# Performance work log

Hardware: AMD Instinct MI355X
Metric: run time of the kernel (lower is better)

Reference implementation:

```python
import jax, jax.numpy as jnp
import numpy as np

N, E = 50000, 800000
IN_C, H_C, OUT_C, HEADS = 64, 32, 32, 8


def setup_inputs() -> dict:
    key = jax.random.key(0)
    ks = jax.random.split(key, 16)
    def glorot(k, shape):
        fan_in = shape[-1]
        return jax.random.normal(k, shape, dtype=jnp.float32) / jnp.sqrt(jnp.float32(fan_in))
    inp = {
        'x': jax.random.normal(ks[0], (N, IN_C), dtype=jnp.float32),
        'edge_index': jax.random.randint(ks[1], (2, E), 0, N, dtype=jnp.int64),
        # layer 1: in_c -> h_c, heads
        'W1l': glorot(ks[2], (HEADS * H_C, IN_C)),
        'b1l': jnp.zeros((HEADS * H_C,), jnp.float32),
        'W1r': glorot(ks[3], (HEADS * H_C, IN_C)),
        'b1r': jnp.zeros((HEADS * H_C,), jnp.float32),
        'att1': glorot(ks[4], (HEADS, H_C)),
        'bias1': jnp.zeros((H_C,), jnp.float32),
        # layer 2: h_c -> out_c, heads
        'W2l': glorot(ks[5], (HEADS * OUT_C, H_C)),
        'b2l': jnp.zeros((HEADS * OUT_C,), jnp.float32),
        'W2r': glorot(ks[6], (HEADS * OUT_C, H_C)),
        'b2r': jnp.zeros((HEADS * OUT_C,), jnp.float32),
        'att2': glorot(ks[7], (HEADS, OUT_C)),
        'bias2': jnp.zeros((OUT_C,), jnp.float32),
    }
    return inp


def _gatv2_layer(x, src, dst, valid, Wl, bl, Wr, br, att, bias):
    # PyG GATv2Conv (share_weights=False, concat=False): message j->i uses
    # e = att . leaky_relu(lin_l(x_j) + lin_r(x_i), 0.2); softmax over dst; agg lin_l(x_j).
    n = x.shape[0]
    heads, c = att.shape
    xl = (x @ Wl.T + bl).reshape(n, heads, c)
    xr = (x @ Wr.T + br).reshape(n, heads, c)
    m = jax.nn.leaky_relu(xl[src] + xr[dst], negative_slope=0.2)  # [Etot,H,C]
    score = jnp.einsum('ehc,hc->eh', m, att)                      # [Etot,H]
    score = jnp.where(valid[:, None], score, -jnp.inf)
    smax = jax.ops.segment_max(score, dst, num_segments=n)        # [N,H]
    a = jnp.where(valid[:, None], jnp.exp(score - smax[dst]), 0.0)
    denom = jax.ops.segment_sum(a, dst, num_segments=n)
    a = a / jnp.maximum(denom[dst], 1e-16)
    out = jax.ops.segment_sum(a[..., None] * xl[src], dst, num_segments=n)  # [N,H,C]
    return out.mean(axis=1) + bias


def reference(x, edge_index, W1l, b1l, W1r, b1r, att1, bias1,
              W2l, b2l, W2r, b2r, att2, bias2):
    n = x.shape[0]
    src0, dst0 = edge_index[0], edge_index[1]
    # PyG removes existing self loops then adds fresh ones: mask originals,
    # append one self loop per node (keeps static shapes).
    loop = jnp.arange(n, dtype=src0.dtype)
    src = jnp.concatenate([src0, loop])
    dst = jnp.concatenate([dst0, loop])
    valid = jnp.concatenate([src0 != dst0, jnp.ones((n,), bool)])
    h = _gatv2_layer(x, src, dst, valid, W1l, b1l, W1r, b1r, att1, bias1)
    h = jax.nn.leaky_relu(h, negative_slope=0.01)  # nn.LeakyReLU default
    out = _gatv2_layer(h, src, dst, valid, W2l, b2l, W2r, b2r, att2, bias2)
    return out
```

## Files before the change

kernel.cpp:

```cpp
#include <hip/hip_runtime.h>
#include <math.h>

#define HEADS 8
#define CDIM 32
#define ODIM 256
#define BKT_SHIFT 7
#define CHUNK 2048

typedef _Float16 h2 __attribute__((ext_vector_type(2)));
typedef _Float16 h4 __attribute__((ext_vector_type(4)));
typedef _Float16 h8 __attribute__((ext_vector_type(8)));
typedef float f32x4 __attribute__((ext_vector_type(4)));
typedef unsigned long long u64;
union H4 { h4 v; h2 p[2]; u64 u; };

#if __has_builtin(__builtin_amdgcn_fdot2)
#define FDOT2(a,b,c) __builtin_amdgcn_fdot2((a),(b),(c),false)
#else
static __device__ __forceinline__ float fdot2_sw(h2 a, h2 b, float c){
  return fmaf((float)a.x, (float)b.x, fmaf((float)a.y, (float)b.y, c));
}
#define FDOT2(a,b,c) fdot2_sw((a),(b),(c))
#endif

__device__ __forceinline__ float lrelu(float v, float s){ return fmaxf(v, s*v); }

__global__ __launch_bounds__(256) void wcvt_kernel(
    const float* __restrict__ W1l, const float* __restrict__ W1r,
    const float* __restrict__ W2l, const float* __restrict__ W2r,
    _Float16* __restrict__ w1lh, _Float16* __restrict__ w1rh,
    _Float16* __restrict__ w2lh, _Float16* __restrict__ w2rh){
  int i = (blockIdx.x*256 + threadIdx.x)*4;
  const float* s; _Float16* d; int off;
  if (i < 16384)      { s = W1l; d = w1lh; off = i; }
  else if (i < 32768) { s = W1r; d = w1rh; off = i - 16384; }
  else if (i < 40960) { s = W2l; d = w2lh; off = i - 32768; }
  else                { s = W2r; d = w2rh; off = i - 40960; }
  float4 v = *(const float4*)(s + off);
  *(h4*)(d + off) = (h4){(_Float16)v.x, (_Float16)v.y, (_Float16)v.z, (_Float16)v.w};
}


__global__ __launch_bounds__(512) void csr_offs_kernel(
    int* __restrict__ hist, int* __restrict__ btotal, int NB, int B){
  __shared__ int s[512];
  int b = blockIdx.x, t = threadIdx.x;
  int v = (t < NB) ? hist[t*B + b] : 0;
  s[t] = v;
  __syncthreads();
  for (int off=1; off<512; off<<=1){
    int u = (t >= off) ? s[t-off] : 0;
    __syncthreads(); s[t] += u; __syncthreads();
  }
  int excl = s[t] - v;
  if (t < NB) hist[t*B + b] = excl;
  if (t == NB-1) btotal[b] = excl + v;
}

__global__ __launch_bounds__(512) void csr_base_kernel(
    const int* __restrict__ btotal, int* __restrict__ base, int B){
  __shared__ int s[512];
  int t = threadIdx.x;
  int v = (t < B) ? btotal[t] : 0;
  s[t] = v;
  __syncthreads();
  for (int off=1; off<512; off<<=1){
    int u = (t >= off) ? s[t-off] : 0;
    __syncthreads(); s[t] += u; __syncthreads();
  }
  if (t < B) base[t] = s[t] - v;
  if (t == B-1) base[B] = s[t];
}

__global__ __launch_bounds__(256) void csr_scatter_kernel(
    const int* __restrict__ src, const int* __restrict__ dst,
    const int* __restrict__ rank, const int* __restrict__ offs,
    const int* __restrict__ base, int* __restrict__ bpack, int e, int B){
  int t = threadIdx.x, k = blockIdx.x;
  int base_i = k*CHUNK;
#pragma unroll
  for (int j = 0; j < CHUNK/256; ++j){
    int i = base_i + j*256 + t;
    if (i < e){
      int r = rank[i];
      if (r >= 0){
        int d = dst[i], s = src[i];
        int b = d >> BKT_SHIFT;
        int pos = base[b] + offs[k*B + b] + r;
        bpack[pos] = (s << BKT_SHIFT) | (d & 127);
      }
    }
  }
}

__global__ __launch_bounds__(256) void csr_sort_kernel(
    const int* __restrict__ bpack, const int* __restrict__ base,
    int* __restrict__ csr, int* __restrict__ indptr, int n, int B){
  __shared__ int lh[128], cur[128], ss[128];
  int b = blockIdx.x, t = threadIdx.x;
  int beg = base[b], cnt = base[b+1] - beg;
  if (t < 128) lh[t] = 0;
  __syncthreads();
  for (int j = t; j < cnt; j += 256){
    int p = bpack[beg + j];
    atomicAdd(&lh[p & 127], 1);
  }
  __syncthreads();
  int v = (t < 128) ? lh[t] : 0;
  if (t < 128) ss[t] = v;
  __syncthreads();
  for (int off=1; off<128; off<<=1){
    int u = (t >= off && t < 128) ? ss[t-off] : 0;
    __syncthreads();
    if (t < 128) ss[t] += u;
    __syncthreads();
  }
  if (t < 128){
    int excl = ss[t] - v;
    cur[t] = excl;
    int node = (b << BKT_SHIFT) + t;
    if (node <= n) indptr[node] = beg + excl;
  }
  __syncthreads();
  for (int j = t; j < cnt; j += 256){
    int p = bpack[beg + j];
    int lpos = atomicAdd(&cur[p & 127], 1);
    csr[beg + lpos] = p >> BKT_SHIFT;
  }
}

template<int K, bool FUSE_HIST>
__global__ __launch_bounds__(512) void gemm_mfma(const float* __restrict__ X,
    const _Float16* __restrict__ Wlh, const float* __restrict__ bl,
    const _Float16* __restrict__ Wrh, const float* __restrict__ br,
    _Float16* __restrict__ outl, _Float16* __restrict__ outr, int n,
    const int* __restrict__ src, const int* __restrict__ dst,
    int* __restrict__ rank, int* __restrict__ hist, int e, int B){
  if (FUSE_HIST && blockIdx.y == 1){
    int k = blockIdx.x;
    int NB = (e + CHUNK-1)/CHUNK;
    if (k >= NB) return;
    __shared__ int lh[512];
    int t = threadIdx.x;
    if (t < 512) lh[t] = 0;
    __syncthreads();
    int base_i = k*CHUNK;
#pragma unroll
    for (int j = 0; j < CHUNK/512; ++j){
      int i = base_i + j*512 + t;
      if (i < e){
        int s = src[i], d = dst[i];
        int r = -1;
        if (s != d) r = atomicAdd(&lh[d>>BKT_SHIFT], 1);
        rank[i] = r;
      }
    }
    __syncthreads();
    for (int b = t; b < B; b += 512) hist[k*B + b] = lh[b];
    return;
  }
  const int KP = K + 8;
  __shared__ __align__(16) _Float16 Xs[64*(K+8)];
  int t = threadIdx.x;
  int n0 = blockIdx.x*64;

  for (int idx = t; idx < 64*(K/4); idx += 512){
    int row = idx/(K/4), c = (idx%(K/4))*4;
    int node = n0 + row; if (node >= n) node = n-1;
    f32x4 xv = __builtin_nontemporal_load((const f32x4*)(X + (size_t)node*K + c));
    *(h4*)(Xs + row*KP + c) = (h4){(_Float16)xv[0], (_Float16)xv[1],
                                   (_Float16)xv[2], (_Float16)xv[3]};
  }
  __syncthreads();

  int wave = t >> 6, lane = t & 63;
  int co = wave*64;
  const _Float16* W = (co < 256) ? Wlh : Wrh;
  const float* Bv   = (co < 256) ? bl : br;
  _Float16* outp    = (co < 256) ? outl : outr;
  int lco = co & 255;
  int lr = lane & 15, lg = lane >> 4;

  f32x4 acc[4][4];
#pragma unroll
  for (int c = 0; c < 4; ++c)
#pragma unroll
    for (int m = 0; m < 4; ++m) acc[c][m] = (f32x4){0.f, 0.f, 0.f, 0.f};

#pragma unroll
  for (int ks = 0; ks < K/32; ++ks){
    int k0 = ks*32 + lg*8;
    h8 a[4], b[4];
#pragma unroll
    for (int c = 0; c < 4; ++c)
      a[c] = *(const h8*)(W + (size_t)(lco + c*16 + lr)*K + k0);
#pragma unroll
    for (int m = 0; m < 4; ++m)
      b[m] = *(const h8*)(Xs + (m*16 + lr)*KP + k0);
#pragma unroll
    for (int c = 0; c < 4; ++c)
#pragma unroll
      for (int m = 0; m < 4; ++m)
        acc[c][m] = __builtin_amdgcn_mfma_f32_16x16x32_f16(a[c], b[m], acc[c][m], 0, 0, 0);
  }

#pragma unroll
  for (int c = 0; c < 4; ++c){
    int ch = lco + c*16 + lg*4;
    float4 bb = *(const float4*)(Bv + ch);
#pragma unroll
    for (int m = 0; m < 4; ++m){
      int node = n0 + m*16 + lr;
      if (node < n){
        h4 o = {(_Float16)(acc[c][m][0] + bb.x), (_Float16)(acc[c][m][1] + bb.y),
                (_Float16)(acc[c][m][2] + bb.z), (_Float16)(acc[c][m][3] + bb.w)};
        *(h4*)(outp + (size_t)node*ODIM + ch) = o;
      }
    }
  }
}

__global__ __launch_bounds__(256) void edge_kernel(
    const _Float16* __restrict__ xl, const _Float16* __restrict__ xr,
    const float* __restrict__ att, const float* __restrict__ bias,
    const int* __restrict__ indptr, const int* __restrict__ csr_src,
    float* __restrict__ out, int n, int act)
{
  int wid = blockIdx.x*4 + (threadIdx.x >> 6);
  if (wid >= n) return;
  int lane = threadIdx.x & 63;
  const float LOG2E = 1.44269504088896341f;

  float4 attf = *(const float4*)(att + 4*lane);
  h2 at0 = (h2){(_Float16)(attf.x*LOG2E), (_Float16)(attf.y*LOG2E)};
  h2 at1 = (h2){(_Float16)(attf.z*LOG2E), (_Float16)(attf.w*LOG2E)};
  const h2 c02 = {(_Float16)0.2f, (_Float16)0.2f};

  H4 xrh; xrh.u = __builtin_nontemporal_load((const u64*)(xr + (size_t)wid*ODIM + 4*lane));
  H4 self; self.v = *(const h4*)(xl + (size_t)wid*ODIM + 4*lane);

  auto score = [&](const H4& c)->float{
    h2 t0 = c.p[0] + xrh.p[0];
    h2 t1 = c.p[1] + xrh.p[1];
    h2 q0 = __builtin_elementwise_max(t0, t0 * c02);
    h2 q1 = __builtin_elementwise_max(t1, t1 * c02);
    float d = FDOT2(q0, at0, FDOT2(q1, at1, 0.f));
    d += __shfl_xor(d, 1);
    d += __shfl_xor(d, 2);
    d += __shfl_xor(d, 4);
    return d;
  };

  float w0 = exp2f(score(self));
  float denom = w0;
  float4 acc;
  acc.x = w0 * (float)self.v.x;
  acc.y = w0 * (float)self.v.y;
  acc.z = w0 * (float)self.v.z;
  acc.w = w0 * (float)self.v.w;

  int beg = __builtin_amdgcn_readfirstlane(indptr[wid]);
  int end = __builtin_amdgcn_readfirstlane(indptr[wid+1]);
  int cnt = end - beg;

#define GATHER(j) (*(const h4*)(xl + (size_t)((unsigned)__shfl(sidx,(j)))*ODIM + 4*lane))
  for (int cb = 0; cb < cnt; cb += 64){
    int ccnt = min(cnt - cb, 64);
    int sidx = (lane < ccnt) ? __builtin_nontemporal_load(csr_src + beg + cb + lane) : 0;
    H4 r0, r1, r2, r3;
    r0.v = (h4){}; r1.v = (h4){}; r2.v = (h4){}; r3.v = (h4){};
    if (ccnt > 0) r0.v = GATHER(0);
    if (ccnt > 1) r1.v = GATHER(1);
    if (ccnt > 2) r2.v = GATHER(2);
    if (ccnt > 3) r3.v = GATHER(3);
#pragma unroll 2
    for (int k = 0; k < ccnt; k += 2){
      H4 e0 = r0, e1 = r1;
      r0 = r2; r1 = r3;
      if (k+4 < ccnt) r2.v = GATHER(k+4);
      if (k+5 < ccnt) r3.v = GATHER(k+5);
      float s0 = score(e0);
      float s1 = score(e1);
      float pe0 = exp2f(s0);
      float pe1 = (k+1 < ccnt) ? exp2f(s1) : 0.f;
      denom += pe0 + pe1;
      acc.x = fmaf(pe0, (float)e0.v.x, fmaf(pe1, (float)e1.v.x, acc.x));
      acc.y = fmaf(pe0, (float)e0.v.y, fmaf(pe1, (float)e1.v.y, acc.y));
      acc.z = fmaf(pe0, (float)e0.v.z, fmaf(pe1, (float)e1.v.z, acc.z));
      acc.w = fmaf(pe0, (float)e0.v.w, fmaf(pe1, (float)e1.v.w, acc.w));
    }
  }
#undef GATHER

  float inv = 1.f/denom;
  float vx = acc.x*inv, vy = acc.y*inv, vz = acc.z*inv, vw = acc.w*inv;
  vx += __shfl_xor(vx, 8);  vx += __shfl_xor(vx, 16);  vx += __shfl_xor(vx, 32);
  vy += __shfl_xor(vy, 8);  vy += __shfl_xor(vy, 16);  vy += __shfl_xor(vy, 32);
  vz += __shfl_xor(vz, 8);  vz += __shfl_xor(vz, 16);  vz += __shfl_xor(vz, 32);
  vw += __shfl_xor(vw, 8);  vw += __shfl_xor(vw, 16);  vw += __shfl_xor(vw, 32);
  if (lane < 8){
    float4 bv = *(const float4*)(bias + 4*lane);
    float ox = vx*0.125f + bv.x;
    float oy = vy*0.125f + bv.y;
    float oz = vz*0.125f + bv.z;
    float ow = vw*0.125f + bv.w;
    if (act){
      ox = lrelu(ox, 0.01f); oy = lrelu(oy, 0.01f);
      oz = lrelu(oz, 0.01f); ow = lrelu(ow, 0.01f);
    }
    f32x4 ov = {ox, oy, oz, ow};
    __builtin_nontemporal_store(ov, (f32x4*)(out + (size_t)wid*CDIM + 4*lane));
  }
}

extern "C" void kernel_launch(void* const* d_in, const int* in_sizes, int n_in,
                              void* d_out, int out_size, void* d_ws, size_t ws_size,
                              hipStream_t stream){
  (void)n_in; (void)out_size; (void)ws_size;
  const float* x    = (const float*)d_in[0];
  const int*   ei   = (const int*)d_in[1];
  const float* W1l  = (const float*)d_in[2];
  const float* b1l  = (const float*)d_in[3];
  const float* W1r  = (const float*)d_in[4];
  const float* b1r  = (const float*)d_in[5];
  const float* att1 = (const float*)d_in[6];
  const float* bias1= (const float*)d_in[7];
  const float* W2l  = (const float*)d_in[8];
  const float* b2l  = (const float*)d_in[9];
  const float* W2r  = (const float*)d_in[10];
  const float* b2r  = (const float*)d_in[11];
  const float* att2 = (const float*)d_in[12];
  const float* bias2= (const float*)d_in[13];
  int n = in_sizes[0] / 64;
  int e = in_sizes[1] / 2;
  const int* src = ei;
  const int* dst = ei + e;

  char* ws = (char*)d_ws;
  size_t off = 0;
  auto alloc = [&](size_t bytes)->char*{
    char* p = ws + off; off += (bytes + 255) & ~(size_t)255; return p;
  };
  _Float16* xl  = (_Float16*)alloc((size_t)n*ODIM*2);
  _Float16* xr  = (_Float16*)alloc((size_t)n*ODIM*2);
  float* h      = (float*)alloc((size_t)n*CDIM*4);
  int*   indptr = (int*)alloc((size_t)(n+1)*4);
  int*   rank   = (int*)alloc((size_t)e*4);
  int*   csr    = (int*)alloc((size_t)e*4);
  int*   bpack  = (int*)alloc((size_t)e*4);
  _Float16* w1lh = (_Float16*)alloc((size_t)ODIM*64*2);
  _Float16* w1rh = (_Float16*)alloc((size_t)ODIM*64*2);
  _Float16* w2lh = (_Float16*)alloc((size_t)ODIM*32*2);
  _Float16* w2rh = (_Float16*)alloc((size_t)ODIM*32*2);

  int NB = (e + CHUNK-1) / CHUNK;
  int B  = (n + 127) >> 7;
  int*   hist   = (int*)alloc((size_t)NB*B*4);
  int*   btotal = (int*)alloc((size_t)B*4);
  int*   base   = (int*)alloc((size_t)(B+1)*4);

  int nt64 = (n + 63) / 64;

  wcvt_kernel<<<48, 256, 0, stream>>>(W1l, W1r, W2l, W2r, w1lh, w1rh, w2lh, w2rh);
  gemm_mfma<64,true><<<dim3(nt64,2), 512, 0, stream>>>(
      x, w1lh, b1l, w1rh, b1r, xl, xr, n, src, dst, rank, hist, e, B);
  csr_offs_kernel<<<B, 512, 0, stream>>>(hist, btotal, NB, B);
  csr_base_kernel<<<1, 512, 0, stream>>>(btotal, base, B);
  csr_scatter_kernel<<<NB, 256, 0, stream>>>(src, dst, rank, hist, base, bpack, e, B);
  csr_sort_kernel<<<B, 256, 0, stream>>>(bpack, base, csr, indptr, n, B);

  edge_kernel<<<(n+3)/4, 256, 0, stream>>>(xl, xr, att1, bias1, indptr, csr, h, n, 1);
  gemm_mfma<32,false><<<dim3(nt64,1), 512, 0, stream>>>(
      h, w2lh, b2l, w2rh, b2r, xl, xr, n, nullptr, nullptr, nullptr, nullptr, 0, 0);
  edge_kernel<<<(n+3)/4, 256, 0, stream>>>(xl, xr, att2, bias2, indptr, csr, (float*)d_out, n, 0);
}
```

Before: 302.7 us.

## Fuse CSR build into one cooperative kernel with fixed-capacity buckets

Replaces four CSR-construction kernels (offset scan, base scan, scatter, per-bucket sort) with a single cooperative kernel that uses grid-wide syncs between phases. Buckets get a fixed capacity of 4096 entries, which removes the global base scan, and edge kernels now read separate begin/end arrays. This is meant to cut launch and inter-kernel gaps, but any bucket holding more than 4096 edges would silently drop edges, and grid.sync adds its own overhead.

```diff
diff --git a/kernel.cpp b/kernel.cpp
--- a/kernel.cpp
+++ b/kernel.cpp
@@ -1,11 +1,15 @@
 #include <hip/hip_runtime.h>
+#include <hip/hip_cooperative_groups.h>
 #include <math.h>
+
+namespace cg = cooperative_groups;
 
 #define HEADS 8
 #define CDIM 32
 #define ODIM 256
 #define BKT_SHIFT 7
 #define CHUNK 2048
+#define CAP 4096
 
 typedef _Float16 h2 __attribute__((ext_vector_type(2)));
 typedef _Float16 h4 __attribute__((ext_vector_type(4)));
@@ -40,92 +44,79 @@
   *(h4*)(d + off) = (h4){(_Float16)v.x, (_Float16)v.y, (_Float16)v.z, (_Float16)v.w};
 }
 
-
-__global__ __launch_bounds__(512) void csr_offs_kernel(
-    int* __restrict__ hist, int* __restrict__ btotal, int NB, int B){
+__global__ __launch_bounds__(512) void coop_csr_kernel(
+    int* __restrict__ hist, int* __restrict__ btotal,
+    const int* __restrict__ src, const int* __restrict__ dst,
+    const int* __restrict__ rank, int* __restrict__ bpack,
+    int* __restrict__ csr, int* __restrict__ ind_beg, int* __restrict__ ind_end,
+    int e, int B, int NB, int n)
+{
+  cg::grid_group grid = cg::this_grid();
+  int blk = blockIdx.x, t = threadIdx.x;
   __shared__ int s[512];
-  int b = blockIdx.x, t = threadIdx.x;
-  int v = (t < NB) ? hist[t*B + b] : 0;
-  s[t] = v;
-  __syncthreads();
-  for (int off=1; off<512; off<<=1){
-    int u = (t >= off) ? s[t-off] : 0;
-    __syncthreads(); s[t] += u; __syncthreads();
-  }
-  int excl = s[t] - v;
-  if (t < NB) hist[t*B + b] = excl;
-  if (t == NB-1) btotal[b] = excl + v;
-}
-
-__global__ __launch_bounds__(512) void csr_base_kernel(
-    const int* __restrict__ btotal, int* __restrict__ base, int B){
-  __shared__ int s[512];
-  int t = threadIdx.x;
-  int v = (t < B) ? btotal[t] : 0;
-  s[t] = v;
-  __syncthreads();
-  for (int off=1; off<512; off<<=1){
-    int u = (t >= off) ? s[t-off] : 0;
-    __syncthreads(); s[t] += u; __syncthreads();
-  }
-  if (t < B) base[t] = s[t] - v;
-  if (t == B-1) base[B] = s[t];
-}
-
-__global__ __launch_bounds__(256) void csr_scatter_kernel(
-    const int* __restrict__ src, const int* __restrict__ dst,
-    const int* __restrict__ rank, const int* __restrict__ offs,
-    const int* __restrict__ base, int* __restrict__ bpack, int e, int B){
-  int t = threadIdx.x, k = blockIdx.x;
-  int base_i = k*CHUNK;
-#pragma unroll
-  for (int j = 0; j < CHUNK/256; ++j){
-    int i = base_i + j*256 + t;
-    if (i < e){
-      int r = rank[i];
-      if (r >= 0){
-        int d = dst[i], s = src[i];
-        int b = d >> BKT_SHIFT;
-        int pos = base[b] + offs[k*B + b] + r;
-        bpack[pos] = (s << BKT_SHIFT) | (d & 127);
+  __shared__ int lh[128], cur[128];
+
+  if (blk < B){
+    int v = (t < NB) ? hist[t*B + blk] : 0;
+    s[t] = v;
+    __syncthreads();
+    for (int off=1; off<512; off<<=1){
+      int u = (t >= off) ? s[t-off] : 0;
+      __syncthreads(); s[t] += u; __syncthreads();
+    }
+    int excl = s[t] - v;
+    if (t < NB) hist[t*B + blk] = excl;
+    if (t == NB-1) btotal[blk] = excl + v;
+  }
+  grid.sync();
+
+  if (blk < NB){
+    int base_i = blk*CHUNK;
+#pragma unroll
+    for (int j = 0; j < CHUNK/512; ++j){
+      int i = base_i + j*512 + t;
+      if (i < e){
+        int r = rank[i];
+        if (r >= 0){
+          int d = dst[i], sv = src[i];
+          int b = d >> BKT_SHIFT;
+          int pos = b*CAP + hist[blk*B + b] + r;
+          bpack[pos] = (sv << BKT_SHIFT) | (d & 127);
+        }
       }
     }
   }
-}
-
-__global__ __launch_bounds__(256) void csr_sort_kernel(
-    const int* __restrict__ bpack, const int* __restrict__ base,
-    int* __restrict__ csr, int* __restrict__ indptr, int n, int B){
-  __shared__ int lh[128], cur[128], ss[128];
-  int b = blockIdx.x, t = threadIdx.x;
-  int beg = base[b], cnt = base[b+1] - beg;
-  if (t < 128) lh[t] = 0;
-  __syncthreads();
-  for (int j = t; j < cnt; j += 256){
-    int p = bpack[beg + j];
-    atomicAdd(&lh[p & 127], 1);
-  }
-  __syncthreads();
-  int v = (t < 128) ? lh[t] : 0;
-  if (t < 128) ss[t] = v;
-  __syncthreads();
-  for (int off=1; off<128; off<<=1){
-    int u = (t >= off && t < 128) ? ss[t-off] : 0;
-    __syncthreads();
-    if (t < 128) ss[t] += u;
-    __syncthreads();
-  }
-  if (t < 128){
-    int excl = ss[t] - v;
-    cur[t] = excl;
-    int node = (b << BKT_SHIFT) + t;
-    if (node <= n) indptr[node] = beg + excl;
-  }
-  __syncthreads();
-  for (int j = t; j < cnt; j += 256){
-    int p = bpack[beg + j];
-    int lpos = atomicAdd(&cur[p & 127], 1);
-    csr[beg + lpos] = p >> BKT_SHIFT;
+  grid.sync();
+
+  if (blk < B){
+    int beg = blk*CAP;
+    int cnt = btotal[blk]; if (cnt > CAP) cnt = CAP;
+    if (t < 128) lh[t] = 0;
+    __syncthreads();
+    for (int j = t; j < cnt; j += 512)
+      atomicAdd(&lh[bpack[beg+j] & 127], 1);
+    __syncthreads();
+    int v = (t < 128) ? lh[t] : 0;
+    if (t < 128) s[t] = v;
+    __syncthreads();
+    for (int off=1; off<128; off<<=1){
+      int u = (t >= off && t < 128) ? s[t-off] : 0;
+      __syncthreads();
+      if (t < 128) s[t] += u;
+      __syncthreads();
+    }
+    if (t < 128){
+      int excl = s[t] - v;
+      cur[t] = excl;
+      int node = (blk << BKT_SHIFT) + t;
+      if (node < n){ ind_beg[node] = beg + excl; ind_end[node] = beg + excl + v; }
+    }
+    __syncthreads();
+    for (int j = t; j < cnt; j += 512){
+      int p = bpack[beg + j];
+      int lpos = atomicAdd(&cur[p & 127], 1);
+      csr[beg + lpos] = p >> BKT_SHIFT;
+    }
   }
 }
 
@@ -223,7 +214,8 @@
 __global__ __launch_bounds__(256) void edge_kernel(
     const _Float16* __restrict__ xl, const _Float16* __restrict__ xr,
     const float* __restrict__ att, const float* __restrict__ bias,
-    const int* __restrict__ indptr, const int* __restrict__ csr_src,
+    const int* __restrict__ ind_beg, const int* __restrict__ ind_end,
+    const int* __restrict__ csr_src,
     float* __restrict__ out, int n, int act)
 {
   int wid = blockIdx.x*4 + (threadIdx.x >> 6);
@@ -259,8 +251,8 @@
   acc.z = w0 * (float)self.v.z;
   acc.w = w0 * (float)self.v.w;
 
-  int beg = __builtin_amdgcn_readfirstlane(indptr[wid]);
-  int end = __builtin_amdgcn_readfirstlane(indptr[wid+1]);
+  int beg = __builtin_amdgcn_readfirstlane(ind_beg[wid]);
+  int end = __builtin_amdgcn_readfirstlane(ind_end[wid]);
   int cnt = end - beg;
 
 #define GATHER(j) (*(const h4*)(xl + (size_t)((unsigned)__shfl(sidx,(j)))*ODIM + 4*lane))
@@ -333,8 +325,8 @@
   const float* bias2= (const float*)d_in[13];
   int n = in_sizes[0] / 64;
   int e = in_sizes[1] / 2;
-  const int* src = ei;
-  const int* dst = ei + e;
+  const int* srcp = ei;
+  const int* dstp = ei + e;
 
   char* ws = (char*)d_ws;
   size_t off = 0;
@@ -344,33 +336,38 @@
   _Float16* xl  = (_Float16*)alloc((size_t)n*ODIM*2);
   _Float16* xr  = (_Float16*)alloc((size_t)n*ODIM*2);
   float* h      = (float*)alloc((size_t)n*CDIM*4);
-  int*   indptr = (int*)alloc((size_t)(n+1)*4);
+  int*   ind_beg = (int*)alloc((size_t)n*4);
+  int*   ind_end = (int*)alloc((size_t)n*4);
   int*   rank   = (int*)alloc((size_t)e*4);
-  int*   csr    = (int*)alloc((size_t)e*4);
-  int*   bpack  = (int*)alloc((size_t)e*4);
+
+  int NB = (e + CHUNK-1) / CHUNK;
+  int B  = (n + 127) >> 7;
+  int*   csr    = (int*)alloc((size_t)B*CAP*4);
+  int*   bpack  = (int*)alloc((size_t)B*CAP*4);
   _Float16* w1lh = (_Float16*)alloc((size_t)ODIM*64*2);
   _Float16* w1rh = (_Float16*)alloc((size_t)ODIM*64*2);
   _Float16* w2lh = (_Float16*)alloc((size_t)ODIM*32*2);
   _Float16* w2rh = (_Float16*)alloc((size_t)ODIM*32*2);
-
-  int NB = (e + CHUNK-1) / CHUNK;
-  int B  = (n + 127) >> 7;
   int*   hist   = (int*)alloc((size_t)NB*B*4);
   int*   btotal = (int*)alloc((size_t)B*4);
-  int*   base   = (int*)alloc((size_t)(B+1)*4);
 
   int nt64 = (n + 63) / 64;
 
   wcvt_kernel<<<48, 256, 0, stream>>>(W1l, W1r, W2l, W2r, w1lh, w1rh, w2lh, w2rh);
   gemm_mfma<64,true><<<dim3(nt64,2), 512, 0, stream>>>(
-      x, w1lh, b1l, w1rh, b1r, xl, xr, n, src, dst, rank, hist, e, B);
-  csr_offs_kernel<<<B, 512, 0, stream>>>(hist, btotal, NB, B);
-  csr_base_kernel<<<1, 512, 0, stream>>>(btotal, base, B);
-  csr_scatter_kernel<<<NB, 256, 0, stream>>>(src, dst, rank, hist, base, bpack, e, B);
-  csr_sort_kernel<<<B, 256, 0, stream>>>(bpack, base, csr, indptr, n, B);
-
-  edge_kernel<<<(n+3)/4, 256, 0, stream>>>(xl, xr, att1, bias1, indptr, csr, h, n, 1);
+      x, w1lh, b1l, w1rh, b1r, xl, xr, n, srcp, dstp, rank, hist, e, B);
+  {
+    void* args[] = {(void*)&hist, (void*)&btotal, (void*)&srcp, (void*)&dstp,
+                    (void*)&rank, (void*)&bpack, (void*)&csr,
+                    (void*)&ind_beg, (void*)&ind_end,
+                    (void*)&e, (void*)&B, (void*)&NB, (void*)&n};
+    int grid = (NB > B) ? NB : B;
+    hipLaunchCooperativeKernel((const void*)coop_csr_kernel,
+                               dim3(grid), dim3(512), args, 0, stream);
+  }
+
+  edge_kernel<<<(n+3)/4, 256, 0, stream>>>(xl, xr, att1, bias1, ind_beg, ind_end, csr, h, n, 1);
   gemm_mfma<32,false><<<dim3(nt64,1), 512, 0, stream>>>(
       h, w2lh, b2l, w2rh, b2r, xl, xr, n, nullptr, nullptr, nullptr, nullptr, 0, 0);
-  edge_kernel<<<(n+3)/4, 256, 0, stream>>>(xl, xr, att2, bias2, indptr, csr, (float*)d_out, n, 0);
-}
+  edge_kernel<<<(n+3)/4, 256, 0, stream>>>(xl, xr, att2, bias2, ind_beg, ind_end, csr, (float*)d_out, n, 0);
+}
```

After: 434.9 us. 1.44x slower.
